# Optimization experiments

Measured on AMD Instinct MI355X. Metric: run time of the kernel, lower is better.

Reference implementation:

```python
import jax, jax.numpy as jnp
import numpy as np

NUM_NODES = 50000
NUM_RELATIONS = 16
NUM_EDGES = 800000
HIDDEN = 64
NUM_CLASSES = 16


def setup_inputs() -> dict:
    key = jax.random.key(0)
    ks = jax.random.split(key, 8)
    edge_index = jax.random.randint(ks[0], (2, NUM_EDGES), 0, NUM_NODES, dtype=jnp.int32)
    edge_type = jax.random.randint(ks[1], (NUM_EDGES,), 0, NUM_RELATIONS, dtype=jnp.int32)
    node_emb = jax.random.normal(ks[2], (NUM_NODES, HIDDEN), dtype=jnp.float32) * 0.1
    W1 = jax.random.normal(ks[3], (NUM_RELATIONS, HIDDEN, HIDDEN), dtype=jnp.float32) * 0.1
    root1 = jax.random.normal(ks[4], (HIDDEN, HIDDEN), dtype=jnp.float32) * 0.1
    b1 = jnp.zeros((HIDDEN,), dtype=jnp.float32)
    W2 = jax.random.normal(ks[5], (NUM_RELATIONS, HIDDEN, NUM_CLASSES), dtype=jnp.float32) * 0.1
    root2 = jax.random.normal(ks[6], (HIDDEN, NUM_CLASSES), dtype=jnp.float32) * 0.1
    b2 = jnp.zeros((NUM_CLASSES,), dtype=jnp.float32)
    return {"edge_index": edge_index, "edge_type": edge_type, "node_emb": node_emb,
            "W1": W1, "root1": root1, "b1": b1, "W2": W2, "root2": root2, "b2": b2}


def rgcn_conv(x, src, dst, edge_type, W, root, bias, num_nodes):
    # PyG RGCNConv (aggr='mean', root_weight=True, bias=True, num_bases=None):
    # per relation r: transform all nodes, gather at src, scatter-MEAN at dst
    # (mean over edges of that relation per target node); sum over relations;
    # then add root transform and bias.
    out_dim = W.shape[-1]

    def body(acc, rw):
        W_r, r = rw
        h = x @ W_r                                   # [N, out]
        mask = (edge_type == r).astype(x.dtype)       # [E]
        msg = h[src] * mask[:, None]                  # [E, out]
        summed = jax.ops.segment_sum(msg, dst, num_segments=num_nodes)  # [N, out]
        cnt = jax.ops.segment_sum(mask, dst, num_segments=num_nodes)    # [N]
        mean = jnp.where(cnt[:, None] > 0, summed / jnp.maximum(cnt, 1.0)[:, None], 0.0)
        return acc + mean, None

    acc0 = jnp.zeros((num_nodes, out_dim), dtype=x.dtype)
    agg, _ = jax.lax.scan(body, acc0, (W, jnp.arange(W.shape[0])))
    return agg + x @ root + bias


def reference(edge_index, edge_type, node_emb, W1, root1, b1, W2, root2, b2):
    src, dst = edge_index[0], edge_index[1]
    n = node_emb.shape[0]
    x = rgcn_conv(node_emb, src, dst, edge_type, W1, root1, b1, n)
    x = jax.nn.relu(x)  # dropout p=0.0 -> identity
    x = rgcn_conv(x, src, dst, edge_type, W2, root2, b2, n)
    return x
```

## Files before the change

### kernel.cpp

```cpp
#include <hip/hip_runtime.h>
#include <hip/hip_bf16.h>

#define N_NODES 50000
#define NREL 16
#define HID 64
#define NCLS 16
#define NBKT (N_NODES * NREL)
#define SB 2048
#define NSB ((NBKT + SB - 1) / SB)
#define TILE 32
#define NTB ((N_NODES + TILE - 1) / TILE)
#define XCHUNKS (N_NODES * HID / 8)
#define W1N (17 * HID * HID)
#define W2N (17 * NCLS * HID)

typedef __attribute__((ext_vector_type(8))) short bf16x8;
typedef __attribute__((ext_vector_type(4))) float f32x4;

static __device__ __forceinline__ unsigned short f2bf(float f) {
    __hip_bfloat16 h = __float2bfloat16(f);
    return *reinterpret_cast<unsigned short*>(&h);
}
static __device__ __forceinline__ float bf2f(unsigned short u) {
    __hip_bfloat16 h;
    *reinterpret_cast<unsigned short*>(&h) = u;
    return __bfloat162float(h);
}


__global__ __launch_bounds__(256) void cvt_k(const float* __restrict__ x,
                                             const float* __restrict__ W1,
                                             const float* __restrict__ root1,
                                             const float* __restrict__ W2,
                                             const float* __restrict__ root2,
                                             ushort* __restrict__ xb,
                                             ushort* __restrict__ WbT1,
                                             ushort* __restrict__ WbT2) {
    int i = blockIdx.x * 256 + threadIdx.x;
    if (i < XCHUNKS) {
        float4 f0 = *(const float4*)(x + (size_t)i * 8);
        float4 f1 = *(const float4*)(x + (size_t)i * 8 + 4);
        bf16x8 o;
        o[0] = (short)f2bf(f0.x); o[1] = (short)f2bf(f0.y);
        o[2] = (short)f2bf(f0.z); o[3] = (short)f2bf(f0.w);
        o[4] = (short)f2bf(f1.x); o[5] = (short)f2bf(f1.y);
        o[6] = (short)f2bf(f1.z); o[7] = (short)f2bf(f1.w);
        *(bf16x8*)(xb + (size_t)i * 8) = o;
    } else {
        int j = i - XCHUNKS;
        if (j < W1N) {
            int t = j >> 12, rem = j & 4095, n = rem >> 6, k = rem & 63;
            float v = (t < 16) ? W1[(size_t)t * HID * HID + k * HID + n]
                               : root1[k * HID + n];
            WbT1[j] = f2bf(v);
        } else {
            int m = j - W1N;
            if (m < W2N) {
                int t = m >> 10, rem = m & 1023, n = rem >> 6, k = rem & 63;
                float v = (t < 16) ? W2[(size_t)t * HID * NCLS + k * NCLS + n]
                                   : root2[k * NCLS + n];
                WbT2[m] = f2bf(v);
            }
        }
    }
}

__global__ __launch_bounds__(256) void rank_k(const int* __restrict__ dstp,
                                              const int* __restrict__ et,
                                              int* __restrict__ bcnt,
                                              int* __restrict__ rank, int E) {
    int i = blockIdx.x * 256 + threadIdx.x;
    if (i < E) {
        int b = dstp[i] * NREL + et[i];
        rank[i] = atomicAdd(&bcnt[b], 1);
    }
}

__global__ __launch_bounds__(256) void scan1_k(const int* __restrict__ bcnt,
                                               int* __restrict__ bsum) {
    int b = blockIdx.x, t = threadIdx.x;
    int base = b * SB + t * 8;
    int s = 0;
#pragma unroll
    for (int j = 0; j < 8; ++j)
        if (base + j < NBKT) s += bcnt[base + j];
#pragma unroll
    for (int off = 1; off < 64; off <<= 1) s += __shfl_xor(s, off, 64);
    __shared__ int ws[4];
    if ((t & 63) == 0) ws[t >> 6] = s;
    __syncthreads();
    if (t == 0) bsum[b] = ws[0] + ws[1] + ws[2] + ws[3];
}

__global__ __launch_bounds__(512) void scan2_k(int* __restrict__ bsum,
                                               int* __restrict__ rstart, int E) {
    __shared__ int ts[512];
    int t = threadIdx.x;
    int v = (t < NSB) ? bsum[t] : 0;
    ts[t] = v;
    __syncthreads();
    int acc = v;
    for (int off = 1; off < 512; off <<= 1) {
        int u = (t >= off) ? ts[t - off] : 0;
        __syncthreads();
        acc += u;
        ts[t] = acc;
        __syncthreads();
    }
    if (t < NSB) bsum[t] = acc - v;
    if (t == 0) rstart[NBKT] = E;
}

__global__ __launch_bounds__(256) void scan3_k(int* __restrict__ bcnt,
                                               const int* __restrict__ bsum) {
    int b = blockIdx.x, t = threadIdx.x;
    int base = b * SB + t * 8;
    int a[8];
    int s = 0;
#pragma unroll
    for (int j = 0; j < 8; ++j) {
        a[j] = (base + j < NBKT) ? bcnt[base + j] : 0;
        s += a[j];
    }
    __shared__ int ts[256];
    ts[t] = s;
    __syncthreads();
    int acc = s;
    for (int off = 1; off < 256; off <<= 1) {
        int u = (t >= off) ? ts[t - off] : 0;
        __syncthreads();
        acc += u;
        ts[t] = acc;
        __syncthreads();
    }
    int run = bsum[b] + (acc - s);
#pragma unroll
    for (int j = 0; j < 8; ++j) {
        if (base + j < NBKT) bcnt[base + j] = run;
        run += a[j];
    }
}

__global__ __launch_bounds__(256) void scat_k(const int* __restrict__ srcp,
                                              const int* __restrict__ dstp,
                                              const int* __restrict__ et,
                                              const int* __restrict__ rank,
                                              const int* __restrict__ rstart,
                                              int2* __restrict__ sedge, int E) {
    int i = blockIdx.x * 256 + threadIdx.x;
    if (i < E) {
        int r = et[i];
        int b = dstp[i] * NREL + r;
        int lo = rstart[b], hi = rstart[b + 1];
        float inv = 1.0f / (float)(hi - lo);
        sedge[lo + rank[i]] = make_int2(srcp[i] | (r << 16), __float_as_int(inv));
    }
}


#define GFLUSH()                                                              \
    {                                                                         \
        bf16x8 o_;                                                            \
        o_[0] = (short)f2bf(acc[0]); o_[1] = (short)f2bf(acc[1]);             \
        o_[2] = (short)f2bf(acc[2]); o_[3] = (short)f2bf(acc[3]);             \
        o_[4] = (short)f2bf(acc[4]); o_[5] = (short)f2bf(acc[5]);             \
        o_[6] = (short)f2bf(acc[6]); o_[7] = (short)f2bf(acc[7]);             \
        *(bf16x8*)(Ab + ((curRel * (TILE * 128) + rowoff) ^ sw)) = o_;        \
        acc[0] = 0.f; acc[1] = 0.f; acc[2] = 0.f; acc[3] = 0.f;               \
        acc[4] = 0.f; acc[5] = 0.f; acc[6] = 0.f; acc[7] = 0.f;               \
    }

#define LOADF(W0, V, DX, JB)                                                  \
    _Pragma("unroll") for (int j8 = 0; j8 < 8; ++j8) {                        \
        W0[j8] = __shfl(DX, gbase + j8, 64);                                  \
        V[j8] = zz;                                                           \
        if ((JB)*8 + j8 < deg)                                                \
            V[j8] = *(const bf16x8*)(xcol + (size_t)(W0[j8] & 0xFFFF) * HID); \
    }

#define CONSUME(W0, DY, V, JB)                                                \
    _Pragma("unroll") for (int j8 = 0; j8 < 8; ++j8) {                        \
        if ((JB)*8 + j8 < deg) {                                              \
            int r_ = (W0[j8] >> 16) & 15;                                     \
            if (r_ != curRel) { GFLUSH(); curRel = r_; }                      \
            float inv_ = __int_as_float(__shfl(DY, gbase + j8, 64));          \
            _Pragma("unroll") for (int q = 0; q < 8; ++q)                     \
                acc[q] = fmaf(inv_, bf2f((unsigned short)V[j8][q]), acc[q]);  \
        }                                                                     \
    }

static __device__ __forceinline__ void gather_tile(char* Ab,
                                                   const ushort* __restrict__ ft,
                                                   const int2* __restrict__ sedge,
                                                   const int* __restrict__ rstart,
                                                   int dst0, int tid) {
    int g = tid >> 3, l8 = tid & 7;
    int lane = tid & 63;
    int gbase = lane & 56;
    int node = dst0 + g;
    bool valid = node < N_NODES;

    int lo = 0, hi = 0;
    if (valid) {
        lo = rstart[node * NREL];
        hi = rstart[node * NREL + NREL];
    }

    int sw = (g & 7) << 4;
    int rowoff = (g << 7) + (l8 << 4);
    const bf16x8 zz = {0, 0, 0, 0, 0, 0, 0, 0};

    int2 d0 = {0, 0}, d1 = {0, 0}, d2 = {0, 0}, d3 = {0, 0};
    int p = lo + l8;
    if (p < hi) d0 = sedge[p];
    if (p + 8 < hi) d1 = sedge[p + 8];
    if (p + 16 < hi) d2 = sedge[p + 16];
    if (p + 24 < hi) d3 = sedge[p + 24];

#pragma unroll
    for (int t = 0; t < 16; ++t)
        *(bf16x8*)(Ab + ((t * (TILE * 128) + rowoff) ^ sw)) = zz;
    {
        bf16x8 v = zz;
        if (valid) v = *(const bf16x8*)(ft + (size_t)node * HID + l8 * 8);
        *(bf16x8*)(Ab + ((16 * (TILE * 128) + rowoff) ^ sw)) = v;
    }

    int deg = hi - lo;
    const ushort* xcol = ft + l8 * 8;
    float acc[8] = {0.f, 0.f, 0.f, 0.f, 0.f, 0.f, 0.f, 0.f};
    int curRel = 0;

    int w0A[8], w0B[8];
    bf16x8 vA[8], vB[8];
    LOADF(w0A, vA, d0.x, 0)
    LOADF(w0B, vB, d1.x, 1)
    __builtin_amdgcn_sched_barrier(0);
    CONSUME(w0A, d0.y, vA, 0)
    LOADF(w0A, vA, d2.x, 2)
    __builtin_amdgcn_sched_barrier(0);
    CONSUME(w0B, d1.y, vB, 1)
    LOADF(w0B, vB, d3.x, 3)
    __builtin_amdgcn_sched_barrier(0);
    CONSUME(w0A, d2.y, vA, 2)
    CONSUME(w0B, d3.y, vB, 3)

    for (int e = lo + 32; e < hi; ++e) {
        int2 m = sedge[e];
        int r = (m.x >> 16) & 15;
        if (r != curRel) {
            GFLUSH();
            curRel = r;
        }
        float inv = __int_as_float(m.y);
        bf16x8 v = *(const bf16x8*)(xcol + (size_t)(m.x & 0xFFFF) * HID);
#pragma unroll
        for (int q = 0; q < 8; ++q)
            acc[q] = fmaf(inv, bf2f((unsigned short)v[q]), acc[q]);
    }
    if (deg > 0) GFLUSH();
}

__global__ __launch_bounds__(256) void fuse1_k(const ushort* __restrict__ xb,
                                               const int2* __restrict__ sedge,
                                               const int* __restrict__ rstart,
                                               const ushort* __restrict__ WbT1,
                                               const float* __restrict__ b1,
                                               ushort* __restrict__ X1b) {
    __shared__ bf16x8 Abuf[17 * TILE * 8];
    char* Ab = (char*)Abuf;
    int tid = threadIdx.x;
    int dst0 = blockIdx.x * TILE;

    gather_tile(Ab, xb, sedge, rstart, dst0, tid);

    int wave = tid >> 6, lane = tid & 63;
    int mr = lane & 15, kq = lane >> 4;
    f32x4 c0 = {0.f, 0.f, 0.f, 0.f}, c1 = {0.f, 0.f, 0.f, 0.f};
    const ushort* wb = WbT1 + (wave * 16 + mr) * HID + kq * 8;
    int sw = (mr & 7) << 4;
    int a00o = ((mr << 7) + (kq << 4)) ^ sw;
    int a01o = ((mr << 7) + 64 + (kq << 4)) ^ sw;
    int a10o = (((16 + mr) << 7) + (kq << 4)) ^ sw;
    int a11o = (((16 + mr) << 7) + 64 + (kq << 4)) ^ sw;

    bf16x8 bk0 = *(const bf16x8*)(wb);
    bf16x8 bk1 = *(const bf16x8*)(wb + 32);
    __syncthreads();

    for (int t = 0; t < 17; ++t) {
        bf16x8 nb0 = bk0, nb1 = bk1;
        if (t < 16) {
            nb0 = *(const bf16x8*)(wb + (t + 1) * 4096);
            nb1 = *(const bf16x8*)(wb + (t + 1) * 4096 + 32);
        }
        const char* At = Ab + t * (TILE * 128);
        bf16x8 a00 = *(const bf16x8*)(At + a00o);
        bf16x8 a01 = *(const bf16x8*)(At + a01o);
        bf16x8 a10 = *(const bf16x8*)(At + a10o);
        bf16x8 a11 = *(const bf16x8*)(At + a11o);
        c0 = __builtin_amdgcn_mfma_f32_16x16x32_bf16(a00, bk0, c0, 0, 0, 0);
        c0 = __builtin_amdgcn_mfma_f32_16x16x32_bf16(a01, bk1, c0, 0, 0, 0);
        c1 = __builtin_amdgcn_mfma_f32_16x16x32_bf16(a10, bk0, c1, 0, 0, 0);
        c1 = __builtin_amdgcn_mfma_f32_16x16x32_bf16(a11, bk1, c1, 0, 0, 0);
        bk0 = nb0;
        bk1 = nb1;
    }
    float bias = b1[wave * 16 + mr];
    int col = wave * 16 + mr;
#pragma unroll
    for (int j = 0; j < 4; ++j) {
        int r0 = dst0 + kq * 4 + j;
        if (r0 < N_NODES)
            X1b[(size_t)r0 * HID + col] = f2bf(fmaxf(c0[j] + bias, 0.f));
        int r1 = r0 + 16;
        if (r1 < N_NODES)
            X1b[(size_t)r1 * HID + col] = f2bf(fmaxf(c1[j] + bias, 0.f));
    }
}

__global__ __launch_bounds__(256) void fuse2_k(const ushort* __restrict__ X1b,
                                               const int2* __restrict__ sedge,
                                               const int* __restrict__ rstart,
                                               const ushort* __restrict__ WbT2,
                                               const float* __restrict__ b2,
                                               float* __restrict__ out) {
    __shared__ bf16x8 Abuf[17 * TILE * 8];
    __shared__ float P[4 * TILE * NCLS];
    char* Ab = (char*)Abuf;
    int tid = threadIdx.x;
    int dst0 = blockIdx.x * TILE;

    gather_tile(Ab, X1b, sedge, rstart, dst0, tid);

    int wave = tid >> 6, lane = tid & 63;
    int mr = lane & 15, kq = lane >> 4;
    f32x4 c0 = {0.f, 0.f, 0.f, 0.f}, c1 = {0.f, 0.f, 0.f, 0.f};
    const ushort* wb = WbT2 + mr * HID + kq * 8;
    int sw = (mr & 7) << 4;
    int a00o = ((mr << 7) + (kq << 4)) ^ sw;
    int a01o = ((mr << 7) + 64 + (kq << 4)) ^ sw;
    int a10o = (((16 + mr) << 7) + (kq << 4)) ^ sw;
    int a11o = (((16 + mr) << 7) + 64 + (kq << 4)) ^ sw;

    bf16x8 bk0 = *(const bf16x8*)(wb + wave * 1024);
    bf16x8 bk1 = *(const bf16x8*)(wb + wave * 1024 + 32);
    __syncthreads();

    for (int t = wave; t < 17; t += 4) {
        bf16x8 nb0 = bk0, nb1 = bk1;
        if (t + 4 < 17) {
            nb0 = *(const bf16x8*)(wb + (t + 4) * 1024);
            nb1 = *(const bf16x8*)(wb + (t + 4) * 1024 + 32);
        }
        const char* At = Ab + t * (TILE * 128);
        bf16x8 a00 = *(const bf16x8*)(At + a00o);
        bf16x8 a01 = *(const bf16x8*)(At + a01o);
        bf16x8 a10 = *(const bf16x8*)(At + a10o);
        bf16x8 a11 = *(const bf16x8*)(At + a11o);
        c0 = __builtin_amdgcn_mfma_f32_16x16x32_bf16(a00, bk0, c0, 0, 0, 0);
        c0 = __builtin_amdgcn_mfma_f32_16x16x32_bf16(a01, bk1, c0, 0, 0, 0);
        c1 = __builtin_amdgcn_mfma_f32_16x16x32_bf16(a10, bk0, c1, 0, 0, 0);
        c1 = __builtin_amdgcn_mfma_f32_16x16x32_bf16(a11, bk1, c1, 0, 0, 0);
        bk0 = nb0;
        bk1 = nb1;
    }
    float* Pw = P + wave * (TILE * NCLS);
#pragma unroll
    for (int j = 0; j < 4; ++j) {
        Pw[(kq * 4 + j) * NCLS + mr] = c0[j];
        Pw[(16 + kq * 4 + j) * NCLS + mr] = c1[j];
    }
    __syncthreads();

    int idx = tid * 2;
    int row = idx >> 4, c = idx & 15;
    float s0 = P[idx] + P[512 + idx] + P[1024 + idx] + P[1536 + idx] + b2[c];
    float s1 = P[idx + 1] + P[512 + idx + 1] + P[1024 + idx + 1] +
               P[1536 + idx + 1] + b2[c + 1];
    if (dst0 + row < N_NODES) {
        float2 o = make_float2(s0, s1);
        *(float2*)(out + (size_t)(dst0 + row) * NCLS + c) = o;
    }
}

extern "C" void kernel_launch(void* const* d_in, const int* in_sizes, int n_in,
                              void* d_out, int out_size, void* d_ws, size_t ws_size,
                              hipStream_t stream) {
    const int* ei    = (const int*)d_in[0];
    const int* et    = (const int*)d_in[1];
    const float* x   = (const float*)d_in[2];
    const float* W1  = (const float*)d_in[3];
    const float* r1  = (const float*)d_in[4];
    const float* b1  = (const float*)d_in[5];
    const float* W2  = (const float*)d_in[6];
    const float* r2  = (const float*)d_in[7];
    const float* b2  = (const float*)d_in[8];
    float* out = (float*)d_out;

    int E = in_sizes[0] / 2;
    const int* srcp = ei;
    const int* dstp = ei + E;

    int*    bcnt  = (int*)d_ws;
    int*    rank  = bcnt + (NBKT + 20);
    int*    bsum  = rank + E;
    int2*   sedge = (int2*)(bsum + 512);
    ushort* WbT1  = (ushort*)(sedge + E);
    ushort* WbT2  = WbT1 + W1N;
    ushort* xb    = WbT2 + W2N;
    ushort* X1b   = xb + (size_t)N_NODES * HID;
    int*    rstart = bcnt;

    hipMemsetAsync(bcnt, 0, (NBKT + 20) * sizeof(int), stream);

    int eb = (E + 255) / 256;
    int cvtThreads = XCHUNKS + W1N + W2N;

    cvt_k<<<(cvtThreads + 255) / 256, 256, 0, stream>>>(x, W1, r1, W2, r2, xb, WbT1, WbT2);
    rank_k<<<eb, 256, 0, stream>>>(dstp, et, bcnt, rank, E);
    scan1_k<<<NSB, 256, 0, stream>>>(bcnt, bsum);
    scan2_k<<<1, 512, 0, stream>>>(bsum, rstart, E);
    scan3_k<<<NSB, 256, 0, stream>>>(bcnt, bsum);
    scat_k<<<eb, 256, 0, stream>>>(srcp, dstp, et, rank, rstart, sedge, E);

    fuse1_k<<<NTB, 256, 0, stream>>>(xb, sedge, rstart, WbT1, b1, X1b);
    fuse2_k<<<NTB, 256, 0, stream>>>(X1b, sedge, rstart, WbT2, b2, out);
}
```

Before: 240.2 us.

## Merge rank and convert kernels; batch-prefetch first 32 edges per node in gather

Combines the edge-ranking atomic kernel and the bf16 conversion kernel into one launch that splits work by block index, removing one kernel launch and its serialization gap. In the gather, each lane now loads 32 edge records redundantly, using a clamped index instead of one strided record per lane plus shuffles, then issues all 32 feature-row loads up front before consuming them. This exposes more memory-level parallelism. It also sets a minimum of two blocks per SM on the fused kernels. The large per-thread register arrays (32 int2 plus 32 bf16x8) risk spills or lower occupancy, and the redundant sedge loads add memory traffic for low-degree nodes.

After: 240.2 us. About the same (+0.0%).

```diff
diff --git a/kernel.cpp b/kernel.cpp
--- a/kernel.cpp
+++ b/kernel.cpp
@@ -28,7 +28,11 @@
 }
 
 
-__global__ __launch_bounds__(256) void cvt_k(const float* __restrict__ x,
+__global__ __launch_bounds__(256) void pre_k(const int* __restrict__ dstp,
+                                             const int* __restrict__ et,
+                                             int* __restrict__ bcnt,
+                                             int* __restrict__ rank, int E,
+                                             const float* __restrict__ x,
                                              const float* __restrict__ W1,
                                              const float* __restrict__ root1,
                                              const float* __restrict__ W2,
@@ -36,7 +40,16 @@
                                              ushort* __restrict__ xb,
                                              ushort* __restrict__ WbT1,
                                              ushort* __restrict__ WbT2) {
-    int i = blockIdx.x * 256 + threadIdx.x;
+    int eb = (E + 255) >> 8;
+    if ((int)blockIdx.x < eb) {
+        int i = blockIdx.x * 256 + threadIdx.x;
+        if (i < E) {
+            int b = dstp[i] * NREL + et[i];
+            rank[i] = atomicAdd(&bcnt[b], 1);
+        }
+        return;
+    }
+    int i = (blockIdx.x - eb) * 256 + threadIdx.x;
     if (i < XCHUNKS) {
         float4 f0 = *(const float4*)(x + (size_t)i * 8);
         float4 f1 = *(const float4*)(x + (size_t)i * 8 + 4);
@@ -65,17 +78,6 @@
     }
 }
 
-__global__ __launch_bounds__(256) void rank_k(const int* __restrict__ dstp,
-                                              const int* __restrict__ et,
-                                              int* __restrict__ bcnt,
-                                              int* __restrict__ rank, int E) {
-    int i = blockIdx.x * 256 + threadIdx.x;
-    if (i < E) {
-        int b = dstp[i] * NREL + et[i];
-        rank[i] = atomicAdd(&bcnt[b], 1);
-    }
-}
-
 __global__ __launch_bounds__(256) void scan1_k(const int* __restrict__ bcnt,
                                                int* __restrict__ bsum) {
     int b = blockIdx.x, t = threadIdx.x;
@@ -170,33 +172,12 @@
         acc[4] = 0.f; acc[5] = 0.f; acc[6] = 0.f; acc[7] = 0.f;               \
     }
 
-#define LOADF(W0, V, DX, JB)                                                  \
-    _Pragma("unroll") for (int j8 = 0; j8 < 8; ++j8) {                        \
-        W0[j8] = __shfl(DX, gbase + j8, 64);                                  \
-        V[j8] = zz;                                                           \
-        if ((JB)*8 + j8 < deg)                                                \
-            V[j8] = *(const bf16x8*)(xcol + (size_t)(W0[j8] & 0xFFFF) * HID); \
-    }
-
-#define CONSUME(W0, DY, V, JB)                                                \
-    _Pragma("unroll") for (int j8 = 0; j8 < 8; ++j8) {                        \
-        if ((JB)*8 + j8 < deg) {                                              \
-            int r_ = (W0[j8] >> 16) & 15;                                     \
-            if (r_ != curRel) { GFLUSH(); curRel = r_; }                      \
-            float inv_ = __int_as_float(__shfl(DY, gbase + j8, 64));          \
-            _Pragma("unroll") for (int q = 0; q < 8; ++q)                     \
-                acc[q] = fmaf(inv_, bf2f((unsigned short)V[j8][q]), acc[q]);  \
-        }                                                                     \
-    }
-
 static __device__ __forceinline__ void gather_tile(char* Ab,
                                                    const ushort* __restrict__ ft,
                                                    const int2* __restrict__ sedge,
                                                    const int* __restrict__ rstart,
                                                    int dst0, int tid) {
     int g = tid >> 3, l8 = tid & 7;
-    int lane = tid & 63;
-    int gbase = lane & 56;
     int node = dst0 + g;
     bool valid = node < N_NODES;
 
@@ -205,17 +186,21 @@
         lo = rstart[node * NREL];
         hi = rstart[node * NREL + NREL];
     }
+    int deg = hi - lo;
+    int base = (deg > 0) ? lo : 0;
+    int last = (deg > 0) ? hi - 1 : 0;
 
     int sw = (g & 7) << 4;
     int rowoff = (g << 7) + (l8 << 4);
     const bf16x8 zz = {0, 0, 0, 0, 0, 0, 0, 0};
 
-    int2 d0 = {0, 0}, d1 = {0, 0}, d2 = {0, 0}, d3 = {0, 0};
-    int p = lo + l8;
-    if (p < hi) d0 = sedge[p];
-    if (p + 8 < hi) d1 = sedge[p + 8];
-    if (p + 16 < hi) d2 = sedge[p + 16];
-    if (p + 24 < hi) d3 = sedge[p + 24];
+    int2 d[32];
+#pragma unroll
+    for (int j = 0; j < 32; ++j) {
+        int idx = base + j;
+        if (idx > last) idx = last;
+        d[j] = sedge[idx];
+    }
 
 #pragma unroll
     for (int t = 0; t < 16; ++t)
@@ -226,24 +211,29 @@
         *(bf16x8*)(Ab + ((16 * (TILE * 128) + rowoff) ^ sw)) = v;
     }
 
-    int deg = hi - lo;
     const ushort* xcol = ft + l8 * 8;
+    bf16x8 v[32];
+#pragma unroll
+    for (int j = 0; j < 32; ++j)
+        v[j] = *(const bf16x8*)(xcol + (size_t)(d[j].x & 0xFFFF) * HID);
+    __builtin_amdgcn_sched_barrier(0);
+
     float acc[8] = {0.f, 0.f, 0.f, 0.f, 0.f, 0.f, 0.f, 0.f};
     int curRel = 0;
-
-    int w0A[8], w0B[8];
-    bf16x8 vA[8], vB[8];
-    LOADF(w0A, vA, d0.x, 0)
-    LOADF(w0B, vB, d1.x, 1)
-    __builtin_amdgcn_sched_barrier(0);
-    CONSUME(w0A, d0.y, vA, 0)
-    LOADF(w0A, vA, d2.x, 2)
-    __builtin_amdgcn_sched_barrier(0);
-    CONSUME(w0B, d1.y, vB, 1)
-    LOADF(w0B, vB, d3.x, 3)
-    __builtin_amdgcn_sched_barrier(0);
-    CONSUME(w0A, d2.y, vA, 2)
-    CONSUME(w0B, d3.y, vB, 3)
+#pragma unroll
+    for (int j = 0; j < 32; ++j) {
+        if (j < deg) {
+            int r_ = (d[j].x >> 16) & 15;
+            if (r_ != curRel) {
+                GFLUSH();
+                curRel = r_;
+            }
+            float inv_ = __int_as_float(d[j].y);
+#pragma unroll
+            for (int q = 0; q < 8; ++q)
+                acc[q] = fmaf(inv_, bf2f((unsigned short)v[j][q]), acc[q]);
+        }
+    }
 
     for (int e = lo + 32; e < hi; ++e) {
         int2 m = sedge[e];
@@ -253,20 +243,20 @@
             curRel = r;
         }
         float inv = __int_as_float(m.y);
-        bf16x8 v = *(const bf16x8*)(xcol + (size_t)(m.x & 0xFFFF) * HID);
+        bf16x8 vv = *(const bf16x8*)(xcol + (size_t)(m.x & 0xFFFF) * HID);
 #pragma unroll
         for (int q = 0; q < 8; ++q)
-            acc[q] = fmaf(inv, bf2f((unsigned short)v[q]), acc[q]);
+            acc[q] = fmaf(inv, bf2f((unsigned short)vv[q]), acc[q]);
     }
     if (deg > 0) GFLUSH();
 }
 
-__global__ __launch_bounds__(256) void fuse1_k(const ushort* __restrict__ xb,
-                                               const int2* __restrict__ sedge,
-                                               const int* __restrict__ rstart,
-                                               const ushort* __restrict__ WbT1,
-                                               const float* __restrict__ b1,
-                                               ushort* __restrict__ X1b) {
+__global__ __launch_bounds__(256, 2) void fuse1_k(const ushort* __restrict__ xb,
+                                                  const int2* __restrict__ sedge,
+                                                  const int* __restrict__ rstart,
+                                                  const ushort* __restrict__ WbT1,
+                                                  const float* __restrict__ b1,
+                                                  ushort* __restrict__ X1b) {
     __shared__ bf16x8 Abuf[17 * TILE * 8];
     char* Ab = (char*)Abuf;
     int tid = threadIdx.x;
@@ -319,12 +309,12 @@
     }
 }
 
-__global__ __launch_bounds__(256) void fuse2_k(const ushort* __restrict__ X1b,
-                                               const int2* __restrict__ sedge,
-                                               const int* __restrict__ rstart,
-                                               const ushort* __restrict__ WbT2,
-                                               const float* __restrict__ b2,
-                                               float* __restrict__ out) {
+__global__ __launch_bounds__(256, 2) void fuse2_k(const ushort* __restrict__ X1b,
+                                                  const int2* __restrict__ sedge,
+                                                  const int* __restrict__ rstart,
+                                                  const ushort* __restrict__ WbT2,
+                                                  const float* __restrict__ b2,
+                                                  float* __restrict__ out) {
     __shared__ bf16x8 Abuf[17 * TILE * 8];
     __shared__ float P[4 * TILE * NCLS];
     char* Ab = (char*)Abuf;
@@ -416,9 +406,10 @@
 
     int eb = (E + 255) / 256;
     int cvtThreads = XCHUNKS + W1N + W2N;
-
-    cvt_k<<<(cvtThreads + 255) / 256, 256, 0, stream>>>(x, W1, r1, W2, r2, xb, WbT1, WbT2);
-    rank_k<<<eb, 256, 0, stream>>>(dstp, et, bcnt, rank, E);
+    int cvtBlocks = (cvtThreads + 255) / 256;
+
+    pre_k<<<eb + cvtBlocks, 256, 0, stream>>>(dstp, et, bcnt, rank, E,
+                                              x, W1, r1, W2, r2, xb, WbT1, WbT2);
     scan1_k<<<NSB, 256, 0, stream>>>(bcnt, bsum);
     scan2_k<<<1, 512, 0, stream>>>(bsum, rstart, E);
     scan3_k<<<NSB, 256, 0, stream>>>(bcnt, bsum);
```
